# Optimization experiments

Measured on AMD Instinct MI355X. Metric: run time of the kernel, lower is better.

Reference implementation:

```python
import jax, jax.numpy as jnp
import numpy as np

B, S, D, H, KH, DH, L, V, MULT = 1, 2048, 2048, 16, 2, 128, 4, 10000, 4
INNER = D * MULT
EPS = 1e-5


def layernorm(x, g, b):
    m = jnp.mean(x, axis=-1, keepdims=True)
    v = jnp.var(x, axis=-1, keepdims=True)
    return (x - m) * jax.lax.rsqrt(v + EPS) * g + b


def setup_inputs() -> dict:
    key = jax.random.key(0)
    ks = jax.random.split(key, 24)
    s = lambda *shape: 0.02
    inp = {
        'text': jax.random.randint(ks[0], (B, S), 0, V),
        'embed_w': jax.random.normal(ks[1], (V, D), jnp.float32) * 0.02,
        # model-level LayerNorm (applied after embed and after every block)
        'model_norm_g': jnp.ones((D,), jnp.float32),
        'model_norm_b': jnp.zeros((D,), jnp.float32),
        # per-block params, stacked on leading L axis
        'blk_norm_g': jnp.ones((L, D), jnp.float32),
        'blk_norm_b': jnp.zeros((L, D), jnp.float32),
        'attn_norm_g': jnp.ones((L, D), jnp.float32),  # RingAttention prenorm
        'attn_norm_b': jnp.zeros((L, D), jnp.float32),
        'wq': jax.random.normal(ks[2], (L, D, H * DH), jnp.float32) * 0.02,
        'wk': jax.random.normal(ks[3], (L, D, KH * DH), jnp.float32) * 0.02,
        'wv': jax.random.normal(ks[4], (L, D, KH * DH), jnp.float32) * 0.02,
        'wo': jax.random.normal(ks[5], (L, H * DH, D), jnp.float32) * 0.02,
        'qn_g': jnp.ones((L, DH), jnp.float32),  # qk_norm LayerNorm scales
        'kn_g': jnp.ones((L, DH), jnp.float32),
        'w1': jax.random.normal(ks[6], (L, D, INNER), jnp.float32) * 0.02,
        'b1': jnp.zeros((L, INNER), jnp.float32),
        'w2': jax.random.normal(ks[7], (L, INNER, D), jnp.float32) * 0.02,
        'b2': jnp.zeros((L, D), jnp.float32),
        # output head: LayerNorm + Linear(D, V)
        'head_norm_g': jnp.ones((D,), jnp.float32),
        'head_norm_b': jnp.zeros((D,), jnp.float32),
        'head_w': jax.random.normal(ks[8], (D, V), jnp.float32) * 0.02,
        'head_b': jnp.zeros((V,), jnp.float32),
    }
    return inp


def _attention(xn, wq, wk, wv, wo, qn_g, kn_g):
    # xn: [B,S,D] (already prenormed)
    q = (xn @ wq).reshape(B, S, H, DH)
    k = (xn @ wk).reshape(B, S, KH, DH)
    v = (xn @ wv).reshape(B, S, KH, DH)
    # qk-norm: LayerNorm over head dim with learnable scale
    q = layernorm(q, qn_g, 0.0)
    k = layernorm(k, kn_g, 0.0)
    # GQA: expand kv heads to query heads
    rep = H // KH
    k = jnp.repeat(k, rep, axis=2)  # [B,S,H,DH]
    v = jnp.repeat(v, rep, axis=2)
    scale = DH ** -0.5
    scores = jnp.einsum('bqhd,bkhd->bhqk', q, k) * scale  # [B,H,S,S]
    causal = jnp.tril(jnp.ones((S, S), bool))
    scores = jnp.where(causal, scores, jnp.finfo(scores.dtype).min)
    p = jax.nn.softmax(scores, axis=-1)
    out = jnp.einsum('bhqk,bkhd->bqhd', p, v).reshape(B, S, H * DH)
    return out @ wo


def reference(text, embed_w, model_norm_g, model_norm_b, blk_norm_g, blk_norm_b,
              attn_norm_g, attn_norm_b, wq, wk, wv, wo, qn_g, kn_g,
              w1, b1, w2, b2, head_norm_g, head_norm_b, head_w, head_b):
    x = embed_w[text]                                # [B,S,D]
    x = layernorm(x, model_norm_g, model_norm_b)
    for i in range(L):
        h = layernorm(x, blk_norm_g[i], blk_norm_b[i])       # block norm
        hn = layernorm(h, attn_norm_g[i], attn_norm_b[i])    # attn prenorm
        h = _attention(hn, wq[i], wk[i], wv[i], wo[i], qn_g[i], kn_g[i]) + h
        ff = jax.nn.gelu(h @ w1[i] + b1[i]) @ w2[i] + b2[i]
        x = ff + h
        x = layernorm(x, model_norm_g, model_norm_b)
    x = layernorm(x, head_norm_g, head_norm_b)
    return x @ head_w + head_b                       # [B,S,V] logits
```

## Files before the change

kernel.cpp:

```cpp
#include <hip/hip_runtime.h>
#include <math.h>

#define S_LEN 2048
#define DMODEL 2048
#define NHEAD 16
#define KVHEAD 2
#define DHEAD 128
#define NLAYER 4
#define VOCAB 10000
#define INNER_DIM 8192
#define LN_EPS 1e-5f
#define VOCAB_PAD 10240
#define QKVN 2560

typedef __attribute__((ext_vector_type(4))) float f32x4;
typedef __attribute__((ext_vector_type(2))) float f32x2;
typedef __attribute__((ext_vector_type(8))) short s16x8;
typedef __attribute__((ext_vector_type(4))) short s16x4;

__device__ __forceinline__ short f2bf(float f) {
  union { float f; unsigned u; } v; v.f = f;
  unsigned r = v.u + 0x7FFFu + ((v.u >> 16) & 1u);
  return (short)(r >> 16);
}
__device__ __forceinline__ float bf2f(short s) {
  union { unsigned u; float f; } v; v.u = ((unsigned)(unsigned short)s) << 16;
  return v.f;
}

__device__ __forceinline__ float gelu_tanh(float x) {
  float z = 0.7978845608028654f * (x + 0.044715f * x * x * x);
  float t = __expf(-2.0f * fabsf(z));
  float th = (1.0f - t) / (1.0f + t);
  th = copysignf(th, z);
  return 0.5f * x * (1.0f + th);
}

__device__ __forceinline__ void glds16(const void* g, void* l) {
  __builtin_amdgcn_global_load_lds(
      (const __attribute__((address_space(1))) unsigned int*)g,
      (__attribute__((address_space(3))) unsigned int*)l, 16, 0, 0);
}

__global__ __launch_bounds__(256)
void wtrans_all(const float* __restrict__ wq, const float* __restrict__ wk,
                const float* __restrict__ wv, const float* __restrict__ wo,
                const float* __restrict__ w1, const float* __restrict__ w2,
                short* __restrict__ wqkvT, short* __restrict__ woT,
                short* __restrict__ w1T, short* __restrict__ w2T) {
  __shared__ float ld[64][65];
  int b = blockIdx.x;
  const float* W; short* WT; int gx, K;
  if (b < 1024)      { W = wq; WT = wqkvT; gx = 32; K = 2048; }
  else if (b < 1152) { b -= 1024; W = wk; WT = wqkvT + (size_t)2048 * 2048; gx = 4; K = 2048; }
  else if (b < 1280) { b -= 1152; W = wv; WT = wqkvT + (size_t)2304 * 2048; gx = 4; K = 2048; }
  else if (b < 2304) { b -= 1280; W = wo; WT = woT; gx = 32; K = 2048; }
  else if (b < 6400) { b -= 2304; W = w1; WT = w1T; gx = 128; K = 2048; }
  else               { b -= 6400; W = w2; WT = w2T; gx = 32; K = 8192; }
  const int N = gx * 64;
  const int n0 = (b % gx) * 64, k0 = (b / gx) * 64;
  const int tid = threadIdx.x;
  const int rbase = tid >> 4;
  const int c4 = (tid & 15) * 4;
#pragma unroll
  for (int q = 0; q < 4; ++q) {
    int kk = rbase + q * 16;
    f32x4 v = *(const f32x4*)(W + (size_t)(k0 + kk) * N + n0 + c4);
    ld[kk][c4 + 0] = v[0]; ld[kk][c4 + 1] = v[1];
    ld[kk][c4 + 2] = v[2]; ld[kk][c4 + 3] = v[3];
  }
  __syncthreads();
#pragma unroll
  for (int s = 0; s < 2; ++s) {
    int lin = tid + s * 256;
    int nn = lin >> 3;
    int ks = lin & 7;
    s16x8 o;
#pragma unroll
    for (int j = 0; j < 8; ++j) o[j] = f2bf(ld[ks * 8 + j][nn]);
    *(s16x8*)&WT[(size_t)(n0 + nn) * K + k0 + ks * 8] = o;
  }
}

__global__ __launch_bounds__(256)
void wtrans64(const float* __restrict__ W, short* __restrict__ WT,
              int K, int N, int NP) {
  __shared__ float ld[64][65];
  const int n0 = blockIdx.x * 64, k0 = blockIdx.y * 64;
  const int tid = threadIdx.x;
  const int rbase = tid >> 4;
  const int c4 = (tid & 15) * 4;
#pragma unroll
  for (int q = 0; q < 4; ++q) {
    int kk = rbase + q * 16;
    const float* wp = W + (size_t)(k0 + kk) * N + n0 + c4;
    float v0, v1, v2, v3;
    if (n0 + c4 + 3 < N) {
      f32x4 v = *(const f32x4*)wp;
      v0 = v[0]; v1 = v[1]; v2 = v[2]; v3 = v[3];
    } else {
      v0 = (n0 + c4 + 0 < N) ? wp[0] : 0.f;
      v1 = (n0 + c4 + 1 < N) ? wp[1] : 0.f;
      v2 = (n0 + c4 + 2 < N) ? wp[2] : 0.f;
      v3 = (n0 + c4 + 3 < N) ? wp[3] : 0.f;
    }
    ld[kk][c4 + 0] = v0; ld[kk][c4 + 1] = v1;
    ld[kk][c4 + 2] = v2; ld[kk][c4 + 3] = v3;
  }
  __syncthreads();
#pragma unroll
  for (int s = 0; s < 2; ++s) {
    int lin = tid + s * 256;
    int nn = lin >> 3;
    int ks = lin & 7;
    int n = n0 + nn;
    if (n < NP) {
      s16x8 o;
#pragma unroll
      for (int j = 0; j < 8; ++j)
        o[j] = (n < N) ? f2bf(ld[ks * 8 + j][nn]) : (short)0;
      *(s16x8*)&WT[(size_t)n * K + k0 + ks * 8] = o;
    }
  }
}

__device__ __forceinline__ void ln3_core(
    float (&v)[8], int tid, int wave,
    const float* __restrict__ mg, const float* __restrict__ mb,
    const float* __restrict__ bg, const float* __restrict__ bb,
    const float* __restrict__ ag, const float* __restrict__ ab,
    float* __restrict__ hbrow, short* __restrict__ hnrow,
    float rs[3][4], float rs2[3][4]) {
#pragma unroll
  for (int rnd = 0; rnd < 3; ++rnd) {
    float s = 0.f, s2 = 0.f;
#pragma unroll
    for (int i = 0; i < 8; ++i) { s += v[i]; s2 += v[i] * v[i]; }
#pragma unroll
    for (int off = 1; off < 64; off <<= 1) {
      s += __shfl_xor(s, off); s2 += __shfl_xor(s2, off);
    }
    if ((tid & 63) == 0) { rs[rnd][wave] = s; rs2[rnd][wave] = s2; }
    __syncthreads();
    s = rs[rnd][0] + rs[rnd][1] + rs[rnd][2] + rs[rnd][3];
    s2 = rs2[rnd][0] + rs2[rnd][1] + rs2[rnd][2] + rs2[rnd][3];
    const float mean = s * (1.f / DMODEL);
    const float var = s2 * (1.f / DMODEL) - mean * mean;
    const float rstd = rsqrtf(var + LN_EPS);
    const float* gg = (rnd == 0) ? mg : (rnd == 1) ? bg : ag;
    const float* bbv = (rnd == 0) ? mb : (rnd == 1) ? bb : ab;
#pragma unroll
    for (int i = 0; i < 8; ++i) {
      int idx = tid + i * 256;
      v[i] = (v[i] - mean) * rstd * gg[idx] + bbv[idx];
    }
    if (rnd == 1) {
#pragma unroll
      for (int i = 0; i < 8; ++i) hbrow[tid + i * 256] = v[i];
    }
  }
#pragma unroll
  for (int i = 0; i < 8; ++i) hnrow[tid + i * 256] = f2bf(v[i]);
}

__global__ __launch_bounds__(256)
void embed_ln3(const int* __restrict__ text, const float* __restrict__ ew,
               const float* __restrict__ mg, const float* __restrict__ mb,
               const float* __restrict__ bg, const float* __restrict__ bb,
               const float* __restrict__ ag, const float* __restrict__ ab,
               float* __restrict__ hb, short* __restrict__ hn16) {
  const int row = blockIdx.x;
  const int tid = threadIdx.x;
  const int wave = tid >> 6;
  __shared__ float rs[3][4], rs2[3][4];
  float v[8];
  const float* x = ew + (size_t)text[row] * DMODEL;
#pragma unroll
  for (int i = 0; i < 8; ++i) v[i] = x[tid + i * 256];
  ln3_core(v, tid, wave, mg, mb, bg, bb, ag, ab,
           hb + (size_t)row * DMODEL, hn16 + (size_t)row * DMODEL, rs, rs2);
}

__global__ __launch_bounds__(256)
void ln_triple_sum(const float* __restrict__ p0, const float* __restrict__ p1,
                   const short* __restrict__ h216, const float* __restrict__ b2,
                   const float* __restrict__ mg, const float* __restrict__ mb,
                   const float* __restrict__ bg, const float* __restrict__ bb,
                   const float* __restrict__ ag, const float* __restrict__ ab,
                   float* __restrict__ hb, short* __restrict__ hn16) {
  const int row = blockIdx.x;
  const int tid = threadIdx.x;
  const int wave = tid >> 6;
  __shared__ float rs[3][4], rs2[3][4];
  float v[8];
  const size_t base = (size_t)row * DMODEL;
#pragma unroll
  for (int i = 0; i < 8; ++i) {
    int idx = tid + i * 256;
    v[i] = p0[base + idx] + p1[base + idx] + b2[idx] + bf2f(h216[base + idx]);
  }
  ln3_core(v, tid, wave, mg, mb, bg, bb, ag, ab,
           hb + base, hn16 + base, rs, rs2);
}

__global__ __launch_bounds__(256)
void ln_dual_sum(const float* __restrict__ p0, const float* __restrict__ p1,
                 const short* __restrict__ h216, const float* __restrict__ b2,
                 const float* __restrict__ mg, const float* __restrict__ mb,
                 const float* __restrict__ hg, const float* __restrict__ hbv,
                 short* __restrict__ out16) {
  const int row = blockIdx.x;
  const int tid = threadIdx.x;
  const int wave = tid >> 6;
  __shared__ float rs[2][4], rs2[2][4];
  float v[8];
  const size_t base = (size_t)row * DMODEL;
#pragma unroll
  for (int i = 0; i < 8; ++i) {
    int idx = tid + i * 256;
    v[i] = p0[base + idx] + p1[base + idx] + b2[idx] + bf2f(h216[base + idx]);
  }
#pragma unroll
  for (int rnd = 0; rnd < 2; ++rnd) {
    float s = 0.f, s2 = 0.f;
#pragma unroll
    for (int i = 0; i < 8; ++i) { s += v[i]; s2 += v[i] * v[i]; }
#pragma unroll
    for (int off = 1; off < 64; off <<= 1) {
      s += __shfl_xor(s, off); s2 += __shfl_xor(s2, off);
    }
    if ((tid & 63) == 0) { rs[rnd][wave] = s; rs2[rnd][wave] = s2; }
    __syncthreads();
    s = rs[rnd][0] + rs[rnd][1] + rs[rnd][2] + rs[rnd][3];
    s2 = rs2[rnd][0] + rs2[rnd][1] + rs2[rnd][2] + rs2[rnd][3];
    const float mean = s * (1.f / DMODEL);
    const float var = s2 * (1.f / DMODEL) - mean * mean;
    const float rstd = rsqrtf(var + LN_EPS);
    const float* gg = (rnd == 0) ? mg : hg;
    const float* bbv = (rnd == 0) ? mb : hbv;
#pragma unroll
    for (int i = 0; i < 8; ++i) {
      int idx = tid + i * 256;
      v[i] = (v[i] - mean) * rstd * gg[idx] + bbv[idx];
    }
  }
  short* o = out16 + base;
#pragma unroll
  for (int i = 0; i < 8; ++i) o[tid + i * 256] = f2bf(v[i]);
}

template<int BM, int BN, int BK, int WM, int WN, int ACT, bool BIAS, bool RES,
         bool WF, bool WB, bool SPLITK>
__global__ __launch_bounds__(WM * WN * 64)
void gemm_db(const short* __restrict__ A, const short* __restrict__ BT,
             const float* __restrict__ bias, const float* __restrict__ res,
             float* __restrict__ Cf, short* __restrict__ Cb,
             int M, int N, int K, int LDA, int LDB) {
  constexpr int THREADS = WM * WN * 64;
  constexpr int MR = BM / WM / 16;
  constexpr int NR = BN / WN / 16;
  constexpr int KH = BK / 32;
  constexpr int SLOTS = BK / 8;
  constexpr int SMASK = SLOTS - 1;
  constexpr int RSH = (SLOTS == 8) ? 0 : 1;
  constexpr int CSH = (SLOTS == 8) ? 3 : 2;
  constexpr int NIA = (BM * BK) / (THREADS * 8);
  constexpr int NIB = (BN * BK) / (THREADS * 8);
  __shared__ short As[2][BM * BK];
  __shared__ short Bs[2][BN * BK];
  const int tid = threadIdx.x;
  const int wave = tid >> 6, lane = tid & 63;
  const int g = lane >> 4, r = lane & 15;
  const int wm = wave / WN, wn = wave % WN;
  const int zoff = SPLITK ? blockIdx.z * K : 0;
  if (SPLITK && WF) Cf += (size_t)blockIdx.z * M * N;

  const int GY = gridDim.y;
  int lin = blockIdx.x + blockIdx.y * gridDim.x;
  int nwg = gridDim.x * GY;
  int sw = ((nwg & 7) == 0) ? ((lin & 7) * (nwg >> 3) + (lin >> 3)) : lin;
  const int bm = (sw % GY) * BM;
  const int bn = (sw / GY) * BN;

  const short* gsrc[NIA + NIB];
  short* ldst[2][NIA + NIB];
#pragma unroll
  for (int i = 0; i < NIA; ++i) {
    int c = i * THREADS + tid;
    int row = c >> CSH;
    int slot = c & SMASK;
    int col = ((slot ^ ((row >> RSH) & SMASK)) << 3);
    gsrc[i] = A + (size_t)(bm + row) * LDA + zoff + col;
    int base = (i * THREADS + (wave << 6)) << 3;
    ldst[0][i] = &As[0][base];
    ldst[1][i] = &As[1][base];
  }
#pragma unroll
  for (int i = 0; i < NIB; ++i) {
    int c = i * THREADS + tid;
    int row = c >> CSH;
    int slot = c & SMASK;
    int col = ((slot ^ ((row >> RSH) & SMASK)) << 3);
    gsrc[NIA + i] = BT + (size_t)(bn + row) * LDB + zoff + col;
    int base = (i * THREADS + (wave << 6)) << 3;
    ldst[0][NIA + i] = &Bs[0][base];
    ldst[1][NIA + i] = &Bs[1][base];
  }

  f32x4 acc[MR][NR] = {};
  const int NT = K / BK;

#pragma unroll
  for (int i = 0; i < NIA + NIB; ++i) glds16(gsrc[i], ldst[0][i]);
  asm volatile("s_waitcnt vmcnt(0)" ::: "memory");
  __syncthreads();

  for (int t = 0; t < NT; ++t) {
    const int cur = t & 1;
    const short* as = As[cur];
    const short* bs = Bs[cur];
    s16x8 bfr[NR][KH], af[(MR > 1) ? MR / 2 : 1][KH];
#pragma unroll
    for (int n = 0; n < NR; ++n) {
      int rr = wn * (NR * 16) + n * 16 + r;
#pragma unroll
      for (int kk = 0; kk < KH; ++kk) {
        int lg = kk * 4 + g;
        bfr[n][kk] = *(const s16x8*)&bs[rr * BK + ((lg ^ ((rr >> RSH) & SMASK)) << 3)];
      }
    }
#pragma unroll
    for (int mm = 0; mm < MR / 2; ++mm) {
      int rr = wm * (MR * 16) + mm * 16 + r;
#pragma unroll
      for (int kk = 0; kk < KH; ++kk) {
        int lg = kk * 4 + g;
        af[mm][kk] = *(const s16x8*)&as[rr * BK + ((lg ^ ((rr >> RSH) & SMASK)) << 3)];
      }
    }
    if (t + 1 < NT) {
#pragma unroll
      for (int i = 0; i < NIA + NIB; ++i) glds16(gsrc[i] + (t + 1) * BK, ldst[cur ^ 1][i]);
    }
    asm volatile("s_waitcnt lgkmcnt(0)" ::: "memory");
    __builtin_amdgcn_sched_barrier(0);
    __builtin_amdgcn_s_setprio(1);
#pragma unroll
    for (int mm = 0; mm < MR / 2; ++mm)
#pragma unroll
      for (int n = 0; n < NR; ++n)
#pragma unroll
        for (int kk = 0; kk < KH; ++kk)
          acc[mm][n] = __builtin_amdgcn_mfma_f32_16x16x32_bf16(af[mm][kk], bfr[n][kk], acc[mm][n], 0, 0, 0);
    __builtin_amdgcn_s_setprio(0);
    __builtin_amdgcn_s_barrier();
#pragma unroll
    for (int mm = 0; mm < MR / 2; ++mm) {
      int rr = wm * (MR * 16) + (MR / 2 + mm) * 16 + r;
#pragma unroll
      for (int kk = 0; kk < KH; ++kk) {
        int lg = kk * 4 + g;
        af[mm][kk] = *(const s16x8*)&as[rr * BK + ((lg ^ ((rr >> RSH) & SMASK)) << 3)];
      }
    }
    asm volatile("s_waitcnt lgkmcnt(0)" ::: "memory");
    __builtin_amdgcn_sched_barrier(0);
    __builtin_amdgcn_s_setprio(1);
#pragma unroll
    for (int mm = 0; mm < MR / 2; ++mm)
#pragma unroll
      for (int n = 0; n < NR; ++n)
#pragma unroll
        for (int kk = 0; kk < KH; ++kk)
          acc[MR / 2 + mm][n] = __builtin_amdgcn_mfma_f32_16x16x32_bf16(af[mm][kk], bfr[n][kk], acc[MR / 2 + mm][n], 0, 0, 0);
    __builtin_amdgcn_s_setprio(0);
    __syncthreads();
  }

#pragma unroll
  for (int m = 0; m < MR; ++m) {
    int row = bm + wm * (MR * 16) + m * 16 + g * 4;
#pragma unroll
    for (int n = 0; n < NR; ++n) {
      int col = bn + wn * (NR * 16) + n * 16 + r;
      if (col < N) {
#pragma unroll
        for (int j = 0; j < 4; ++j) {
          float v = acc[m][n][j];
          if (BIAS) v += bias[col];
          if (ACT) v = gelu_tanh(v);
          if (RES) v += res[(size_t)(row + j) * N + col];
          if (WF) Cf[(size_t)(row + j) * N + col] = v;
          if (WB) Cb[(size_t)(row + j) * N + col] = f2bf(v);
        }
      }
    }
  }
}

__global__ __launch_bounds__(256)
void gemm_qkv(const short* __restrict__ A, const short* __restrict__ BT,
              const float* __restrict__ qg, const float* __restrict__ kg,
              short* __restrict__ qb, short* __restrict__ kb,
              short* __restrict__ vt, int M, int K) {
  __shared__ short As[2][128 * 64];
  __shared__ short Bs[2][128 * 64];
  __shared__ float rsm[2][128], rs2m[2][128];
  const int tid = threadIdx.x;
  const int wave = tid >> 6, lane = tid & 63;
  const int g = lane >> 4, r = lane & 15;
  const int wm = wave >> 1, wn = wave & 1;

  const int GY = gridDim.y;
  int lin = blockIdx.x + blockIdx.y * gridDim.x;
  int nwg = gridDim.x * GY;
  int sw = (lin & 7) * (nwg >> 3) + (lin >> 3);
  const int bm = (sw % GY) * 128;
  const int bn = (sw / GY) * 128;

  const short* gsrc[8];
  short* ldst[2][8];
#pragma unroll
  for (int i = 0; i < 4; ++i) {
    int c = i * 256 + tid;
    int row = c >> 3;
    int slot = c & 7;
    int col = ((slot ^ (row & 7)) << 3);
    gsrc[i] = A + (size_t)(bm + row) * K + col;
    gsrc[4 + i] = BT + (size_t)(bn + row) * K + col;
    int base = (i * 256 + (wave << 6)) << 3;
    ldst[0][i] = &As[0][base]; ldst[0][4 + i] = &Bs[0][base];
    ldst[1][i] = &As[1][base]; ldst[1][4 + i] = &Bs[1][base];
  }

  f32x4 acc[4][4] = {};
  const int NT = K >> 6;

#pragma unroll
  for (int i = 0; i < 8; ++i) glds16(gsrc[i], ldst[0][i]);
  asm volatile("s_waitcnt vmcnt(0)" ::: "memory");
  __syncthreads();

  for (int t = 0; t < NT; ++t) {
    const int cur = t & 1;
    const short* as = As[cur];
    const short* bs = Bs[cur];
    s16x8 bfr[4][2], af[2][2];
#pragma unroll
    for (int n = 0; n < 4; ++n) {
      int rr = wn * 64 + n * 16 + r;
#pragma unroll
      for (int kk = 0; kk < 2; ++kk) {
        int lg = kk * 4 + g;
        bfr[n][kk] = *(const s16x8*)&bs[rr * 64 + ((lg ^ (rr & 7)) << 3)];
      }
    }
#pragma unroll
    for (int mm = 0; mm < 2; ++mm) {
      int rr = wm * 64 + mm * 16 + r;
#pragma unroll
      for (int kk = 0; kk < 2; ++kk) {
        int lg = kk * 4 + g;
        af[mm][kk] = *(const s16x8*)&as[rr * 64 + ((lg ^ (rr & 7)) << 3)];
      }
    }
    if (t + 1 < NT) {
#pragma unroll
      for (int i = 0; i < 8; ++i) glds16(gsrc[i] + (t + 1) * 64, ldst[cur ^ 1][i]);
    }
    asm volatile("s_waitcnt lgkmcnt(0)" ::: "memory");
    __builtin_amdgcn_sched_barrier(0);
    __builtin_amdgcn_s_setprio(1);
#pragma unroll
    for (int mm = 0; mm < 2; ++mm)
#pragma unroll
      for (int n = 0; n < 4; ++n)
#pragma unroll
        for (int kk = 0; kk < 2; ++kk)
          acc[mm][n] = __builtin_amdgcn_mfma_f32_16x16x32_bf16(af[mm][kk], bfr[n][kk], acc[mm][n], 0, 0, 0);
    __builtin_amdgcn_s_setprio(0);
    __builtin_amdgcn_s_barrier();
#pragma unroll
    for (int mm = 0; mm < 2; ++mm) {
      int rr = wm * 64 + (2 + mm) * 16 + r;
#pragma unroll
      for (int kk = 0; kk < 2; ++kk) {
        int lg = kk * 4 + g;
        af[mm][kk] = *(const s16x8*)&as[rr * 64 + ((lg ^ (rr & 7)) << 3)];
      }
    }
    asm volatile("s_waitcnt lgkmcnt(0)" ::: "memory");
    __builtin_amdgcn_sched_barrier(0);
    __builtin_amdgcn_s_setprio(1);
#pragma unroll
    for (int mm = 0; mm < 2; ++mm)
#pragma unroll
      for (int n = 0; n < 4; ++n)
#pragma unroll
        for (int kk = 0; kk < 2; ++kk)
          acc[2 + mm][n] = __builtin_amdgcn_mfma_f32_16x16x32_bf16(af[mm][kk], bfr[n][kk], acc[2 + mm][n], 0, 0, 0);
    __builtin_amdgcn_s_setprio(0);
    __syncthreads();
  }

  if (bn >= 2304) {
    short* ld = &As[0][0];
#pragma unroll
    for (int m = 0; m < 4; ++m) {
      int sl = wm * 64 + m * 16 + g * 4;
#pragma unroll
      for (int n = 0; n < 4; ++n) {
        int dl = wn * 64 + n * 16 + r;
#pragma unroll
        for (int j = 0; j < 4; ++j)
          ld[(sl + j) * 128 + dl] = f2bf(acc[m][n][j]);
      }
    }
    __syncthreads();
    const int dl = tid & 127;
    const int sh = (tid >> 7) * 64;
    short* dst = vt + (size_t)(bn - 2304 + dl) * S_LEN + bm + sh;
#pragma unroll
    for (int v = 0; v < 8; ++v) {
      s16x8 o;
#pragma unroll
      for (int i = 0; i < 8; ++i) o[i] = ld[(sh + v * 8 + i) * 128 + dl];
      *(s16x8*)(dst + v * 8) = o;
    }
  } else {
    float ms[4][4], m2[4][4];
#pragma unroll
    for (int m = 0; m < 4; ++m)
#pragma unroll
      for (int j = 0; j < 4; ++j) {
        float s = 0.f, s2 = 0.f;
#pragma unroll
        for (int n = 0; n < 4; ++n) { float v = acc[m][n][j]; s += v; s2 += v * v; }
#pragma unroll
        for (int off = 1; off < 16; off <<= 1) {
          s += __shfl_xor(s, off); s2 += __shfl_xor(s2, off);
        }
        ms[m][j] = s; m2[m][j] = s2;
      }
    if (r == 0) {
#pragma unroll
      for (int m = 0; m < 4; ++m)
#pragma unroll
        for (int j = 0; j < 4; ++j) {
          int rl = wm * 64 + m * 16 + g * 4 + j;
          rsm[wn][rl] = ms[m][j]; rs2m[wn][rl] = m2[m][j];
        }
    }
    __syncthreads();
    const float* gv = (bn < 2048) ? qg : kg;
#pragma unroll
    for (int m = 0; m < 4; ++m)
#pragma unroll
      for (int j = 0; j < 4; ++j) {
        int rl = wm * 64 + m * 16 + g * 4 + j;
        float s = rsm[0][rl] + rsm[1][rl];
        float s2 = rs2m[0][rl] + rs2m[1][rl];
        float mean = s * (1.f / 128.f);
        float var = s2 * (1.f / 128.f) - mean * mean;
        float rstd = rsqrtf(var + LN_EPS);
        int srow = bm + rl;
#pragma unroll
        for (int n = 0; n < 4; ++n) {
          int cl = wn * 64 + n * 16 + r;
          float v = (acc[m][n][j] - mean) * rstd * gv[cl];
          if (bn < 2048) qb[(size_t)srow * 2048 + bn + cl] = f2bf(v);
          else kb[(size_t)srow * 256 + (bn - 2048) + cl] = f2bf(v);
        }
      }
  }
}

__global__ __launch_bounds__(256)
void attn_fwd3(const short* __restrict__ qbuf, const short* __restrict__ kbuf,
               const short* __restrict__ vtb, short* __restrict__ obuf) {
  __shared__ short Qs[64 * 128];
  __shared__ short Ks[64 * 128];
  __shared__ short Vt[128 * 64];
  __shared__ short Ps[4][16][88];
  const int tid = threadIdx.x;
  int lin = blockIdx.x + blockIdx.y * gridDim.x;
  int sw = (lin & 7) * 32 + (lin >> 3);
  const int pair = sw & 15;
  const int h = sw >> 4;
  const int kh = h >> 3;
  const int wave = tid >> 6, lane = tid & 63;
  const int g = lane >> 4, r = lane & 15;
  const float scale = 0.08838834764831845f;

#pragma unroll
  for (int half = 0; half < 2; ++half) {
    const int qt = half ? (31 - pair) : pair;
    const int qbase = qt * 64;
    __builtin_amdgcn_s_barrier();
#pragma unroll
    for (int i = 0; i < 4; ++i) {
      int c = i * 256 + tid;
      int row = c >> 4;
      int scol = (((c & 15) ^ (row & 7)) << 3);
      glds16(qbuf + (size_t)(qbase + row) * DMODEL + h * DHEAD + scol,
             &Qs[(i * 256 + (wave << 6)) << 3]);
    }
    f32x4 O[8] = {};
    float mst[4], lst[4];
#pragma unroll
    for (int j = 0; j < 4; ++j) { mst[j] = -1e30f; lst[j] = 0.f; }
    s16x8 aq[4];

    for (int jt = 0; jt <= qt; ++jt) {
      const int jb = jt * 64;
      if (jt) __builtin_amdgcn_s_barrier();
#pragma unroll
      for (int i = 0; i < 4; ++i) {
        int c = i * 256 + tid;
        int row = c >> 4;
        int scol = (((c & 15) ^ (row & 7)) << 3);
        glds16(kbuf + (size_t)(jb + row) * 256 + kh * DHEAD + scol,
               &Ks[(i * 256 + (wave << 6)) << 3]);
      }
#pragma unroll
      for (int i = 0; i < 4; ++i) {
        int c = i * 256 + tid;
        int row = c >> 3;
        int scol = (((c & 7) ^ (row & 7)) << 3);
        glds16(vtb + (size_t)(kh * 128 + row) * S_LEN + jb + scol,
               &Vt[(i * 256 + (wave << 6)) << 3]);
      }
      asm volatile("s_waitcnt vmcnt(4)" ::: "memory");
      __builtin_amdgcn_s_barrier();
      if (jt == 0) {
#pragma unroll
        for (int kc = 0; kc < 4; ++kc) {
          int rr = wave * 16 + r;
          aq[kc] = *(const s16x8*)&Qs[rr * 128 + ((((kc << 2) | g) ^ (rr & 7)) << 3)];
        }
      }
      f32x4 sc[4] = {};
      __builtin_amdgcn_s_setprio(1);
#pragma unroll
      for (int n = 0; n < 4; ++n) {
        int rr = n * 16 + r;
#pragma unroll
        for (int kc = 0; kc < 4; ++kc) {
          s16x8 bk = *(const s16x8*)&Ks[rr * 128 + ((((kc << 2) | g) ^ (rr & 7)) << 3)];
          sc[n] = __builtin_amdgcn_mfma_f32_16x16x32_bf16(aq[kc], bk, sc[n], 0, 0, 0);
        }
      }
      __builtin_amdgcn_s_setprio(0);
      if (jt == qt) {
#pragma unroll
        for (int j = 0; j < 4; ++j) {
          int irow = qbase + wave * 16 + g * 4 + j;
#pragma unroll
          for (int n = 0; n < 4; ++n) {
            int jcol = jb + n * 16 + r;
            sc[n][j] = (jcol <= irow) ? sc[n][j] * scale : -1e30f;
          }
        }
      } else {
#pragma unroll
        for (int j = 0; j < 4; ++j)
#pragma unroll
          for (int n = 0; n < 4; ++n) sc[n][j] *= scale;
      }
      float pmax[4], alpha[4], rsum[4];
#pragma unroll
      for (int j = 0; j < 4; ++j)
        pmax[j] = fmaxf(fmaxf(sc[0][j], sc[1][j]), fmaxf(sc[2][j], sc[3][j]));
#pragma unroll
      for (int off = 1; off < 16; off <<= 1)
#pragma unroll
        for (int j = 0; j < 4; ++j) pmax[j] = fmaxf(pmax[j], __shfl_xor(pmax[j], off));
#pragma unroll
      for (int j = 0; j < 4; ++j) {
        float mnew = fmaxf(mst[j], pmax[j]);
        alpha[j] = __expf(mst[j] - mnew);
        mst[j] = mnew;
#pragma unroll
        for (int n = 0; n < 4; ++n) sc[n][j] = __expf(sc[n][j] - mnew);
        rsum[j] = (sc[0][j] + sc[1][j]) + (sc[2][j] + sc[3][j]);
      }
#pragma unroll
      for (int off = 1; off < 16; off <<= 1)
#pragma unroll
        for (int j = 0; j < 4; ++j) rsum[j] += __shfl_xor(rsum[j], off);
#pragma unroll
      for (int j = 0; j < 4; ++j) lst[j] = lst[j] * alpha[j] + rsum[j];
#pragma unroll
      for (int d = 0; d < 8; ++d)
#pragma unroll
        for (int j = 0; j < 4; ++j) O[d][j] *= alpha[j];
      asm volatile("s_waitcnt vmcnt(0)" ::: "memory");
      __builtin_amdgcn_s_barrier();
#pragma unroll
      for (int j = 0; j < 4; ++j)
#pragma unroll
        for (int n = 0; n < 4; ++n)
          Ps[wave][g * 4 + j][n * 16 + r] = f2bf(sc[n][j]);
      s16x8 pa0 = *(const s16x8*)&Ps[wave][r][g * 8];
      s16x8 pa1 = *(const s16x8*)&Ps[wave][r][32 + g * 8];
      __builtin_amdgcn_s_setprio(1);
#pragma unroll
      for (int d = 0; d < 8; ++d) {
        int dd = d * 16 + r;
        s16x8 b0 = *(const s16x8*)&Vt[dd * 64 + ((g ^ (dd & 7)) << 3)];
        s16x8 b1 = *(const s16x8*)&Vt[dd * 64 + (((4 + g) ^ (dd & 7)) << 3)];
        O[d] = __builtin_amdgcn_mfma_f32_16x16x32_bf16(pa0, b0, O[d], 0, 0, 0);
        O[d] = __builtin_amdgcn_mfma_f32_16x16x32_bf16(pa1, b1, O[d], 0, 0, 0);
      }
      __builtin_amdgcn_s_setprio(0);
    }
    float linv[4];
#pragma unroll
    for (int j = 0; j < 4; ++j) linv[j] = 1.f / lst[j];
#pragma unroll
    for (int d = 0; d < 8; ++d)
#pragma unroll
      for (int j = 0; j < 4; ++j)
        obuf[(size_t)(qbase + wave * 16 + g * 4 + j) * DMODEL + h * DHEAD + d * 16 + r] =
            f2bf(O[d][j] * linv[j]);
  }
}

extern "C" void kernel_launch(void* const* d_in, const int* in_sizes, int n_in,
                              void* d_out, int out_size, void* d_ws, size_t ws_size,
                              hipStream_t stream) {
  const int* text = (const int*)d_in[0];
  const float* embed_w = (const float*)d_in[1];
  const float* model_g = (const float*)d_in[2];
  const float* model_b = (const float*)d_in[3];
  const float* blk_g = (const float*)d_in[4];
  const float* blk_b = (const float*)d_in[5];
  const float* attn_g = (const float*)d_in[6];
  const float* attn_b = (const float*)d_in[7];
  const float* wq = (const float*)d_in[8];
  const float* wk = (const float*)d_in[9];
  const float* wv = (const float*)d_in[10];
  const float* wo = (const float*)d_in[11];
  const float* qn_g = (const float*)d_in[12];
  const float* kn_g = (const float*)d_in[13];
  const float* w1 = (const float*)d_in[14];
  const float* b1 = (const float*)d_in[15];
  const float* w2 = (const float*)d_in[16];
  const float* b2 = (const float*)d_in[17];
  const float* head_g = (const float*)d_in[18];
  const float* head_b = (const float*)d_in[19];
  const float* head_w = (const float*)d_in[20];
  const float* head_bias = (const float*)d_in[21];
  float* out = (float*)d_out;

  const size_t SD = (size_t)S_LEN * DMODEL;
  const size_t SKV = (size_t)S_LEN * KVHEAD * DHEAD;
  const size_t SI = (size_t)S_LEN * INNER_DIM;
  const size_t WD = (size_t)DMODEL * DMODEL;
  const size_t WKV = (size_t)DMODEL * KVHEAD * DHEAD;
  const size_t WI = (size_t)DMODEL * INNER_DIM;

  char* p = (char*)d_ws;
  float* hb    = (float*)p; p += SD * 4;
  float* wpart = (float*)p; p += SD * 4 * 2;
  short* hn16  = (short*)p; p += SD * 2;
  short* h216  = (short*)p; p += SD * 2;
  short* ao16  = (short*)p; p += SD * 2;
  short* ffi16 = (short*)p; p += SI * 2;
  short* qb16  = (short*)p; p += SD * 2;
  short* kb16  = (short*)p; p += SKV * 2;
  short* vt16  = (short*)p; p += SKV * 2;
  short* wqkvT = (short*)p; p += (size_t)QKVN * DMODEL * 2;
  short* woT   = (short*)p; p += WD * 2;
  short* w1T   = (short*)p; p += WI * 2;
  short* w2T   = (short*)p; p += WI * 2;
  short* headT = w1T;

  dim3 blk(256);
  embed_ln3<<<S_LEN, blk, 0, stream>>>(text, embed_w, model_g, model_b,
                                       blk_g, blk_b, attn_g, attn_b, hb, hn16);

  for (int i = 0; i < NLAYER; ++i) {
    wtrans_all<<<10496, blk, 0, stream>>>(
        wq + (size_t)i * WD, wk + (size_t)i * WKV, wv + (size_t)i * WKV,
        wo + (size_t)i * WD, w1 + (size_t)i * WI, w2 + (size_t)i * WI,
        wqkvT, woT, w1T, w2T);

    gemm_qkv<<<dim3(QKVN / 128, S_LEN / 128), blk, 0, stream>>>(
        hn16, wqkvT, qn_g + i * DHEAD, kn_g + i * DHEAD,
        qb16, kb16, vt16, S_LEN, DMODEL);

    attn_fwd3<<<dim3(16, 16), blk, 0, stream>>>(qb16, kb16, vt16, ao16);

    gemm_db<64, 128, 64, 2, 2, 0, false, true, false, true, false>
        <<<dim3(DMODEL / 128, S_LEN / 64), blk, 0, stream>>>(
        ao16, woT, nullptr, hb, nullptr, h216,
        S_LEN, DMODEL, DMODEL, DMODEL, DMODEL);
    gemm_db<128, 128, 64, 2, 2, 1, true, false, false, true, false>
        <<<dim3(INNER_DIM / 128, S_LEN / 128), blk, 0, stream>>>(
        h216, w1T, b1 + (size_t)i * INNER_DIM, nullptr, nullptr, ffi16,
        S_LEN, INNER_DIM, DMODEL, DMODEL, DMODEL);
    gemm_db<128, 128, 64, 2, 2, 0, false, false, true, false, true>
        <<<dim3(DMODEL / 128, S_LEN / 128, 2), blk, 0, stream>>>(
        ffi16, w2T, nullptr, nullptr, wpart, nullptr,
        S_LEN, DMODEL, INNER_DIM / 2, INNER_DIM, INNER_DIM);

    if (i + 1 < NLAYER) {
      ln_triple_sum<<<S_LEN, blk, 0, stream>>>(
          wpart, wpart + SD, h216, b2 + (size_t)i * DMODEL,
          model_g, model_b,
          blk_g + (i + 1) * DMODEL, blk_b + (i + 1) * DMODEL,
          attn_g + (i + 1) * DMODEL, attn_b + (i + 1) * DMODEL, hb, hn16);
    } else {
      ln_dual_sum<<<S_LEN, blk, 0, stream>>>(
          wpart, wpart + SD, h216, b2 + (size_t)i * DMODEL,
          model_g, model_b, head_g, head_b, hn16);
    }
  }

  wtrans64<<<dim3(VOCAB_PAD / 64, 32), blk, 0, stream>>>(head_w, headT, DMODEL, VOCAB, VOCAB_PAD);
  gemm_db<128, 128, 64, 2, 2, 0, true, false, true, false, false>
      <<<dim3(VOCAB_PAD / 128, S_LEN / 128), blk, 0, stream>>>(
      hn16, headT, head_bias, nullptr, out, nullptr,
      S_LEN, VOCAB, DMODEL, DMODEL, DMODEL);
}
```

Baseline: 1.489 ms.

## Store residual stream in bf16 and halve QKV GEMM row tile

```diff
diff --git a/kernel.cpp b/kernel.cpp
--- a/kernel.cpp
+++ b/kernel.cpp
@@ -129,7 +129,7 @@
     const float* __restrict__ mg, const float* __restrict__ mb,
     const float* __restrict__ bg, const float* __restrict__ bb,
     const float* __restrict__ ag, const float* __restrict__ ab,
-    float* __restrict__ hbrow, short* __restrict__ hnrow,
+    short* __restrict__ hbrow, short* __restrict__ hnrow,
     float rs[3][4], float rs2[3][4]) {
 #pragma unroll
   for (int rnd = 0; rnd < 3; ++rnd) {
@@ -156,7 +156,7 @@
     }
     if (rnd == 1) {
 #pragma unroll
-      for (int i = 0; i < 8; ++i) hbrow[tid + i * 256] = v[i];
+      for (int i = 0; i < 8; ++i) hbrow[tid + i * 256] = f2bf(v[i]);
     }
   }
 #pragma unroll
@@ -168,7 +168,7 @@
                const float* __restrict__ mg, const float* __restrict__ mb,
                const float* __restrict__ bg, const float* __restrict__ bb,
                const float* __restrict__ ag, const float* __restrict__ ab,
-               float* __restrict__ hb, short* __restrict__ hn16) {
+               short* __restrict__ hb16, short* __restrict__ hn16) {
   const int row = blockIdx.x;
   const int tid = threadIdx.x;
   const int wave = tid >> 6;
@@ -178,7 +178,7 @@
 #pragma unroll
   for (int i = 0; i < 8; ++i) v[i] = x[tid + i * 256];
   ln3_core(v, tid, wave, mg, mb, bg, bb, ag, ab,
-           hb + (size_t)row * DMODEL, hn16 + (size_t)row * DMODEL, rs, rs2);
+           hb16 + (size_t)row * DMODEL, hn16 + (size_t)row * DMODEL, rs, rs2);
 }
 
 __global__ __launch_bounds__(256)
@@ -187,7 +187,7 @@
                    const float* __restrict__ mg, const float* __restrict__ mb,
                    const float* __restrict__ bg, const float* __restrict__ bb,
                    const float* __restrict__ ag, const float* __restrict__ ab,
-                   float* __restrict__ hb, short* __restrict__ hn16) {
+                   short* __restrict__ hb16, short* __restrict__ hn16) {
   const int row = blockIdx.x;
   const int tid = threadIdx.x;
   const int wave = tid >> 6;
@@ -200,7 +200,7 @@
     v[i] = p0[base + idx] + p1[base + idx] + b2[idx] + bf2f(h216[base + idx]);
   }
   ln3_core(v, tid, wave, mg, mb, bg, bb, ag, ab,
-           hb + base, hn16 + base, rs, rs2);
+           hb16 + base, hn16 + base, rs, rs2);
 }
 
 __global__ __launch_bounds__(256)
@@ -249,11 +249,11 @@
   for (int i = 0; i < 8; ++i) o[tid + i * 256] = f2bf(v[i]);
 }
 
-template<int BM, int BN, int BK, int WM, int WN, int ACT, bool BIAS, bool RES,
+template<int BM, int BN, int BK, int WM, int WN, int ACT, bool BIAS, bool RESB,
          bool WF, bool WB, bool SPLITK>
 __global__ __launch_bounds__(WM * WN * 64)
 void gemm_db(const short* __restrict__ A, const short* __restrict__ BT,
-             const float* __restrict__ bias, const float* __restrict__ res,
+             const float* __restrict__ bias, const short* __restrict__ res16,
              float* __restrict__ Cf, short* __restrict__ Cb,
              int M, int N, int K, int LDA, int LDB) {
   constexpr int THREADS = WM * WN * 64;
@@ -389,7 +389,7 @@
           float v = acc[m][n][j];
           if (BIAS) v += bias[col];
           if (ACT) v = gelu_tanh(v);
-          if (RES) v += res[(size_t)(row + j) * N + col];
+          if (RESB) v += bf2f(res16[(size_t)(row + j) * N + col]);
           if (WF) Cf[(size_t)(row + j) * N + col] = v;
           if (WB) Cb[(size_t)(row + j) * N + col] = f2bf(v);
         }
@@ -403,9 +403,9 @@
               const float* __restrict__ qg, const float* __restrict__ kg,
               short* __restrict__ qb, short* __restrict__ kb,
               short* __restrict__ vt, int M, int K) {
-  __shared__ short As[2][128 * 64];
+  __shared__ short As[2][64 * 64];
   __shared__ short Bs[2][128 * 64];
-  __shared__ float rsm[2][128], rs2m[2][128];
+  __shared__ float rsm[2][64], rs2m[2][64];
   const int tid = threadIdx.x;
   const int wave = tid >> 6, lane = tid & 63;
   const int g = lane >> 4, r = lane & 15;
@@ -415,29 +415,37 @@
   int lin = blockIdx.x + blockIdx.y * gridDim.x;
   int nwg = gridDim.x * GY;
   int sw = (lin & 7) * (nwg >> 3) + (lin >> 3);
-  const int bm = (sw % GY) * 128;
+  const int bm = (sw % GY) * 64;
   const int bn = (sw / GY) * 128;
 
-  const short* gsrc[8];
-  short* ldst[2][8];
+  const short* gsrc[6];
+  short* ldst[2][6];
+#pragma unroll
+  for (int i = 0; i < 2; ++i) {
+    int c = i * 256 + tid;
+    int row = c >> 3, slot = c & 7;
+    int col = ((slot ^ (row & 7)) << 3);
+    gsrc[i] = A + (size_t)(bm + row) * K + col;
+    int base = (i * 256 + (wave << 6)) << 3;
+    ldst[0][i] = &As[0][base];
+    ldst[1][i] = &As[1][base];
+  }
 #pragma unroll
   for (int i = 0; i < 4; ++i) {
     int c = i * 256 + tid;
-    int row = c >> 3;
-    int slot = c & 7;
+    int row = c >> 3, slot = c & 7;
     int col = ((slot ^ (row & 7)) << 3);
-    gsrc[i] = A + (size_t)(bm + row) * K + col;
-    gsrc[4 + i] = BT + (size_t)(bn + row) * K + col;
+    gsrc[2 + i] = BT + (size_t)(bn + row) * K + col;
     int base = (i * 256 + (wave << 6)) << 3;
-    ldst[0][i] = &As[0][base]; ldst[0][4 + i] = &Bs[0][base];
-    ldst[1][i] = &As[1][base]; ldst[1][4 + i] = &Bs[1][base];
-  }
-
-  f32x4 acc[4][4] = {};
+    ldst[0][2 + i] = &Bs[0][base];
+    ldst[1][2 + i] = &Bs[1][base];
+  }
+
+  f32x4 acc[2][4] = {};
   const int NT = K >> 6;
 
 #pragma unroll
-  for (int i = 0; i < 8; ++i) glds16(gsrc[i], ldst[0][i]);
+  for (int i = 0; i < 6; ++i) glds16(gsrc[i], ldst[0][i]);
   asm volatile("s_waitcnt vmcnt(0)" ::: "memory");
   __syncthreads();
 
@@ -445,7 +453,7 @@
     const int cur = t & 1;
     const short* as = As[cur];
     const short* bs = Bs[cur];
-    s16x8 bfr[4][2], af[2][2];
+    s16x8 bfr[4][2], af[1][2];
 #pragma unroll
     for (int n = 0; n < 4; ++n) {
       int rr = wn * 64 + n * 16 + r;
@@ -455,50 +463,44 @@
         bfr[n][kk] = *(const s16x8*)&bs[rr * 64 + ((lg ^ (rr & 7)) << 3)];
       }
     }
-#pragma unroll
-    for (int mm = 0; mm < 2; ++mm) {
-      int rr = wm * 64 + mm * 16 + r;
+    {
+      int rr = wm * 32 + r;
 #pragma unroll
       for (int kk = 0; kk < 2; ++kk) {
         int lg = kk * 4 + g;
-        af[mm][kk] = *(const s16x8*)&as[rr * 64 + ((lg ^ (rr & 7)) << 3)];
+        af[0][kk] = *(const s16x8*)&as[rr * 64 + ((lg ^ (rr & 7)) << 3)];
       }
     }
     if (t + 1 < NT) {
 #pragma unroll
-      for (int i = 0; i < 8; ++i) glds16(gsrc[i] + (t + 1) * 64, ldst[cur ^ 1][i]);
+      for (int i = 0; i < 6; ++i) glds16(gsrc[i] + (t + 1) * 64, ldst[cur ^ 1][i]);
     }
     asm volatile("s_waitcnt lgkmcnt(0)" ::: "memory");
     __builtin_amdgcn_sched_barrier(0);
     __builtin_amdgcn_s_setprio(1);
 #pragma unroll
-    for (int mm = 0; mm < 2; ++mm)
-#pragma unroll
-      for (int n = 0; n < 4; ++n)
-#pragma unroll
-        for (int kk = 0; kk < 2; ++kk)
-          acc[mm][n] = __builtin_amdgcn_mfma_f32_16x16x32_bf16(af[mm][kk], bfr[n][kk], acc[mm][n], 0, 0, 0);
+    for (int n = 0; n < 4; ++n)
+#pragma unroll
+      for (int kk = 0; kk < 2; ++kk)
+        acc[0][n] = __builtin_amdgcn_mfma_f32_16x16x32_bf16(af[0][kk], bfr[n][kk], acc[0][n], 0, 0, 0);
     __builtin_amdgcn_s_setprio(0);
     __builtin_amdgcn_s_barrier();
-#pragma unroll
-    for (int mm = 0; mm < 2; ++mm) {
-      int rr = wm * 64 + (2 + mm) * 16 + r;
+    {
+      int rr = wm * 32 + 16 + r;
 #pragma unroll
       for (int kk = 0; kk < 2; ++kk) {
         int lg = kk * 4 + g;
-        af[mm][kk] = *(const s16x8*)&as[rr * 64 + ((lg ^ (rr & 7)) << 3)];
+        af[0][kk] = *(const s16x8*)&as[rr * 64 + ((lg ^ (rr & 7)) << 3)];
       }
     }
     asm volatile("s_waitcnt lgkmcnt(0)" ::: "memory");
     __builtin_amdgcn_sched_barrier(0);
     __builtin_amdgcn_s_setprio(1);
 #pragma unroll
-    for (int mm = 0; mm < 2; ++mm)
-#pragma unroll
-      for (int n = 0; n < 4; ++n)
-#pragma unroll
-        for (int kk = 0; kk < 2; ++kk)
-          acc[2 + mm][n] = __builtin_amdgcn_mfma_f32_16x16x32_bf16(af[mm][kk], bfr[n][kk], acc[2 + mm][n], 0, 0, 0);
+    for (int n = 0; n < 4; ++n)
+#pragma unroll
+      for (int kk = 0; kk < 2; ++kk)
+        acc[1][n] = __builtin_amdgcn_mfma_f32_16x16x32_bf16(af[0][kk], bfr[n][kk], acc[1][n], 0, 0, 0);
     __builtin_amdgcn_s_setprio(0);
     __syncthreads();
   }
@@ -506,8 +508,8 @@
   if (bn >= 2304) {
     short* ld = &As[0][0];
 #pragma unroll
-    for (int m = 0; m < 4; ++m) {
-      int sl = wm * 64 + m * 16 + g * 4;
+    for (int m = 0; m < 2; ++m) {
+      int sl = wm * 32 + m * 16 + g * 4;
 #pragma unroll
       for (int n = 0; n < 4; ++n) {
         int dl = wn * 64 + n * 16 + r;
@@ -518,19 +520,19 @@
     }
     __syncthreads();
     const int dl = tid & 127;
-    const int sh = (tid >> 7) * 64;
+    const int sh = (tid >> 7) * 32;
     short* dst = vt + (size_t)(bn - 2304 + dl) * S_LEN + bm + sh;
 #pragma unroll
-    for (int v = 0; v < 8; ++v) {
+    for (int v = 0; v < 4; ++v) {
       s16x8 o;
 #pragma unroll
       for (int i = 0; i < 8; ++i) o[i] = ld[(sh + v * 8 + i) * 128 + dl];
       *(s16x8*)(dst + v * 8) = o;
     }
   } else {
-    float ms[4][4], m2[4][4];
-#pragma unroll
-    for (int m = 0; m < 4; ++m)
+    float ms[2][4], m2[2][4];
+#pragma unroll
+    for (int m = 0; m < 2; ++m)
 #pragma unroll
       for (int j = 0; j < 4; ++j) {
         float s = 0.f, s2 = 0.f;
@@ -544,20 +546,20 @@
       }
     if (r == 0) {
 #pragma unroll
-      for (int m = 0; m < 4; ++m)
+      for (int m = 0; m < 2; ++m)
 #pragma unroll
         for (int j = 0; j < 4; ++j) {
-          int rl = wm * 64 + m * 16 + g * 4 + j;
+          int rl = wm * 32 + m * 16 + g * 4 + j;
           rsm[wn][rl] = ms[m][j]; rs2m[wn][rl] = m2[m][j];
         }
     }
     __syncthreads();
     const float* gv = (bn < 2048) ? qg : kg;
 #pragma unroll
-    for (int m = 0; m < 4; ++m)
+    for (int m = 0; m < 2; ++m)
 #pragma unroll
       for (int j = 0; j < 4; ++j) {
-        int rl = wm * 64 + m * 16 + g * 4 + j;
+        int rl = wm * 32 + m * 16 + g * 4 + j;
         float s = rsm[0][rl] + rsm[1][rl];
         float s2 = rs2m[0][rl] + rs2m[1][rl];
         float mean = s * (1.f / 128.f);
@@ -761,8 +763,8 @@
   const size_t WI = (size_t)DMODEL * INNER_DIM;
 
   char* p = (char*)d_ws;
-  float* hb    = (float*)p; p += SD * 4;
   float* wpart = (float*)p; p += SD * 4 * 2;
+  short* hb16  = (short*)p; p += SD * 2;
   short* hn16  = (short*)p; p += SD * 2;
   short* h216  = (short*)p; p += SD * 2;
   short* ao16  = (short*)p; p += SD * 2;
@@ -778,7 +780,7 @@
 
   dim3 blk(256);
   embed_ln3<<<S_LEN, blk, 0, stream>>>(text, embed_w, model_g, model_b,
-                                       blk_g, blk_b, attn_g, attn_b, hb, hn16);
+                                       blk_g, blk_b, attn_g, attn_b, hb16, hn16);
 
   for (int i = 0; i < NLAYER; ++i) {
     wtrans_all<<<10496, blk, 0, stream>>>(
@@ -786,7 +788,7 @@
         wo + (size_t)i * WD, w1 + (size_t)i * WI, w2 + (size_t)i * WI,
         wqkvT, woT, w1T, w2T);
 
-    gemm_qkv<<<dim3(QKVN / 128, S_LEN / 128), blk, 0, stream>>>(
+    gemm_qkv<<<dim3(QKVN / 128, S_LEN / 64), blk, 0, stream>>>(
         hn16, wqkvT, qn_g + i * DHEAD, kn_g + i * DHEAD,
         qb16, kb16, vt16, S_LEN, DMODEL);
 
@@ -794,7 +796,7 @@
 
     gemm_db<64, 128, 64, 2, 2, 0, false, true, false, true, false>
         <<<dim3(DMODEL / 128, S_LEN / 64), blk, 0, stream>>>(
-        ao16, woT, nullptr, hb, nullptr, h216,
+        ao16, woT, nullptr, hb16, nullptr, h216,
         S_LEN, DMODEL, DMODEL, DMODEL, DMODEL);
     gemm_db<128, 128, 64, 2, 2, 1, true, false, false, true, false>
         <<<dim3(INNER_DIM / 128, S_LEN / 128), blk, 0, stream>>>(
@@ -810,7 +812,7 @@
           wpart, wpart + SD, h216, b2 + (size_t)i * DMODEL,
           model_g, model_b,
           blk_g + (i + 1) * DMODEL, blk_b + (i + 1) * DMODEL,
-          attn_g + (i + 1) * DMODEL, attn_b + (i + 1) * DMODEL, hb, hn16);
+          attn_g + (i + 1) * DMODEL, attn_b + (i + 1) * DMODEL, hb16, hn16);
     } else {
       ln_dual_sum<<<S_LEN, blk, 0, stream>>>(
           wpart, wpart + SD, h216, b2 + (size_t)i * DMODEL,
```

Measured after the change: 1.476 ms, median of 2. No clear change (-0.9%).
